# Kernel tuning notes

Measured on AMD Instinct MI355X. Metric: run time of the kernel, lower is better.

Reference implementation:

```python
import jax, jax.numpy as jnp
import numpy as np

STEP = 2
NEG = -1.0e10  # matches masked_fill_(-10000000000.0)


def leaky_relu(x):
    # nn.LeakyReLU(0.2)
    return jnp.where(x >= 0, x, 0.2 * x)


def setup_inputs() -> dict:
    key = jax.random.key(0)
    k1, k2, k3, k4 = jax.random.split(key, 4)
    B, E, N, H = 16, 1024, 1024, 128
    nodes_hidden = jax.random.normal(k1, (B, N, H), dtype=jnp.float32)
    # sparse-ish binary hyperedge incidence matrix (batch, edge_num, node_num)
    hn_adj = jax.random.bernoulli(k2, 0.1, (B, E, N)).astype(jnp.float32)
    # Linear(H+1, 1, bias=False) weights for q1 / q2, flattened to (H+1,)
    w1 = jax.random.normal(k3, (H + 1,), dtype=jnp.float32) / np.sqrt(H + 1).astype(np.float32)
    w2 = jax.random.normal(k4, (H + 1,), dtype=jnp.float32) / np.sqrt(H + 1).astype(np.float32)
    return {"nodes_hidden": nodes_hidden, "hn_adj": hn_adj, "w1": w1, "w2": w2}


def reference(nodes_hidden, hn_adj, w1, w2):
    # Dropout is inference-mode identity.
    H = nodes_hidden.shape[-1]
    # edge init: mean of incident node features
    deg = jnp.sum(hn_adj, axis=-1, keepdims=True)            # (B,E,1)
    deg = jnp.where(deg == 0.0, 1.0, deg)
    edge = jnp.matmul(hn_adj, nodes_hidden) / deg            # (B,E,H)
    nodes = nodes_hidden
    for _ in range(STEP):
        # q1(concat(edge*node, adj)) == (edge*node)@w1[:H] + adj*w1[H]
        # fused rank-1 score: never materialize (B,E,N,H)
        alpha = leaky_relu(
            jnp.einsum("bed,bnd,d->ben", edge, nodes, w1[:H]) + hn_adj * w1[H]
        )                                                     # (B,E,N)
        alpha = jnp.where(hn_adj == 0, NEG, alpha)
        alpha = jax.nn.softmax(alpha, axis=-1)
        edge = jnp.einsum("ben,bnd->bed", alpha, nodes)       # new edge hidden
        adj_t = jnp.swapaxes(hn_adj, 1, 2)                    # (B,N,E)
        beta = leaky_relu(
            jnp.einsum("bed,bnd,d->bne", edge, nodes, w2[:H]) + adj_t * w2[H]
        )                                                     # (B,N,E)
        beta = jnp.where(adj_t == 0, NEG, beta)
        beta = jax.nn.softmax(beta, axis=-1)
        nodes = jnp.einsum("bne,bed->bnd", beta, edge)        # new node hidden
    return (nodes, edge)
```

## Files before the change

kernel.cpp:

```cpp
#include <hip/hip_runtime.h>
#include <cstdint>
#include <cstddef>

#define B_ 16
#define E_ 1024
#define N_ 1024
#define H_ 128
#define CAP 192
#define NC 16
#define EC 64

typedef unsigned short u16;

#define UPK2(u, flo, fhi) \
    flo = __uint_as_float((u) << 16); fhi = __uint_as_float((u) & 0xffff0000u)

__device__ __forceinline__ u16 f2bf(float f) {
    unsigned u = __float_as_uint(f);
    return (u16)((u + 0x7fffu + ((u >> 16) & 1u)) >> 16);
}

__device__ __forceinline__ float wave_sum64(float v) {
    v += __shfl_xor(v, 32);
    v += __shfl_xor(v, 16);
    v += __shfl_xor(v, 8);
    v += __shfl_xor(v, 4);
    v += __shfl_xor(v, 2);
    v += __shfl_xor(v, 1);
    return v;
}

__global__ void build_rows(const float* __restrict__ adj,
                           u16* __restrict__ idx, int* __restrict__ cnt_out) {
    int be = blockIdx.x;
    const float* row = adj + (size_t)be * N_;
    __shared__ int wcnt[4];
    __shared__ int base;
    int tid = threadIdx.x, lane = tid & 63, wv = tid >> 6;
    if (tid == 0) base = 0;
    __syncthreads();
    for (int c0 = 0; c0 < N_; c0 += 256) {
        float v = row[c0 + tid];
        unsigned long long m = __ballot(v != 0.0f);
        if (lane == 0) wcnt[wv] = __popcll(m);
        __syncthreads();
        int pos = base;
        for (int w = 0; w < wv; ++w) pos += wcnt[w];
        pos += __popcll(m & ((1ull << lane) - 1ull));
        if (v != 0.0f && pos < CAP)
            idx[(size_t)be * CAP + pos] = (u16)(c0 + tid);
        __syncthreads();
        if (tid == 0) base += wcnt[0] + wcnt[1] + wcnt[2] + wcnt[3];
        __syncthreads();
    }
    if (tid == 0) cnt_out[be] = base < CAP ? base : CAP;
}

__global__ void col_count(const float* __restrict__ adj, int* __restrict__ cnt_chunk) {
    int blk = blockIdx.x;
    int ng = blk & 3;
    int c  = (blk >> 2) & (NC - 1);
    int b  = blk >> 6;
    int n = (ng << 8) + threadIdx.x;
    const float* base = adj + ((size_t)(b * E_ + c * EC)) * N_ + n;
    int cc = 0;
#pragma unroll 8
    for (int e = 0; e < EC; ++e)
        cc += (base[(size_t)e * N_] != 0.0f);
    cnt_chunk[(size_t)(b * NC + c) * N_ + n] = cc;
}

__global__ void col_prefix(const int* __restrict__ cnt_chunk,
                           int* __restrict__ off_chunk, int* __restrict__ cnt_out) {
    int idx = blockIdx.x * 256 + threadIdx.x;
    int b = idx >> 10, n = idx & 1023;
    int run = 0;
    for (int c = 0; c < NC; ++c) {
        size_t p = (size_t)(b * NC + c) * N_ + n;
        off_chunk[p] = run;
        run += cnt_chunk[p];
    }
    cnt_out[idx] = run < CAP ? run : CAP;
}

__global__ void col_place(const float* __restrict__ adj,
                          const int* __restrict__ off_chunk, u16* __restrict__ idx) {
    int blk = blockIdx.x;
    int ng = blk & 3;
    int c  = (blk >> 2) & (NC - 1);
    int b  = blk >> 6;
    int n = (ng << 8) + threadIdx.x;
    const float* base = adj + ((size_t)(b * E_ + c * EC)) * N_ + n;
    int pos = off_chunk[(size_t)(b * NC + c) * N_ + n];
    u16* lst = idx + ((size_t)b * N_ + n) * CAP;
    for (int e = 0; e < EC; ++e) {
        if (base[(size_t)e * N_] != 0.0f) {
            if (pos < CAP) lst[pos] = (u16)(c * EC + e);
            ++pos;
        }
    }
}

__global__ void to_bf16(const float* __restrict__ in, u16* __restrict__ out) {
    int i = blockIdx.x * 256 + threadIdx.x;
    float4 v = ((const float4*)in)[i];
    ushort4 r;
    r.x = f2bf(v.x); r.y = f2bf(v.y); r.z = f2bf(v.z); r.w = f2bf(v.w);
    ((ushort4*)out)[i] = r;
}

__global__ void edge_init(const u16* __restrict__ nodes_bf,
                          const u16* __restrict__ ridx, const int* __restrict__ rcnt,
                          float* __restrict__ edge) {
    int be = blockIdx.x;
    int b = be >> 10;
    int tid = threadIdx.x, d4 = tid & 31, h = tid >> 5;
    __shared__ u16 sidx[CAP];
    __shared__ float4 part4[256];
    int cnt = rcnt[be];
    for (int i = tid; i < cnt; i += 256) sidx[i] = ridx[(size_t)be * CAP + i];
    __syncthreads();
    const uint2* nb2 = (const uint2*)(nodes_bf + (size_t)b * N_ * H_);
    float4 acc = make_float4(0.f, 0.f, 0.f, 0.f);
    for (int i = h; i < cnt; i += 8) {
        uint2 u = nb2[(unsigned)sidx[i] * 32 + d4];
        float f0, f1, f2, f3;
        UPK2(u.x, f0, f1); UPK2(u.y, f2, f3);
        acc.x += f0; acc.y += f1; acc.z += f2; acc.w += f3;
    }
    part4[tid] = acc;
    __syncthreads();
    if (tid < 32) {
        float4 r = make_float4(0.f, 0.f, 0.f, 0.f);
#pragma unroll
        for (int k = 0; k < 8; ++k) {
            float4 p = part4[tid + (k << 5)];
            r.x += p.x; r.y += p.y; r.z += p.z; r.w += p.w;
        }
        float inv = 1.0f / (float)(cnt > 0 ? cnt : 1);
        r.x *= inv; r.y *= inv; r.z *= inv; r.w *= inv;
        ((float4*)edge)[(size_t)be * 32 + tid] = r;
    }
}

__global__ void __launch_bounds__(256, 4)
attn_gather(const float* __restrict__ qsrc,
            const u16* __restrict__ kv_bf,
            const float* __restrict__ w,
            const u16* __restrict__ lidx, const int* __restrict__ lcnt,
            float* __restrict__ out, u16* __restrict__ out_bf) {
    int x = blockIdx.x;
    int xcd = x & 7;
    int j = x >> 3;
    int b = xcd + ((j >> 8) << 3);
    int rg = (j & 255) << 2;
    int tid = threadIdx.x, lane = tid & 63, wv = tid >> 6;
    int br = (b << 10) + rg + wv;
    __shared__ u16 sidx[4][CAP];
    int cnt = lcnt[br];
    for (int i = lane; i < cnt; i += 64) sidx[wv][i] = lidx[(size_t)br * CAP + i];

    int esub = lane >> 3, dsub = lane & 7;
    const float4* qp = (const float4*)(qsrc + (size_t)br * H_);
    const float4* wp = (const float4*)w;
    float4 qr0, qr1, qr2, qr3;
    {
        float4 q0 = qp[(dsub << 2) + 0], w0 = wp[(dsub << 2) + 0];
        float4 q1 = qp[(dsub << 2) + 1], w1 = wp[(dsub << 2) + 1];
        float4 q2 = qp[(dsub << 2) + 2], w2 = wp[(dsub << 2) + 2];
        float4 q3 = qp[(dsub << 2) + 3], w3 = wp[(dsub << 2) + 3];
        const float L2E = 1.44269504f;
        qr0.x = q0.x * w0.x * L2E; qr0.y = q0.y * w0.y * L2E;
        qr0.z = q0.z * w0.z * L2E; qr0.w = q0.w * w0.w * L2E;
        qr1.x = q1.x * w1.x * L2E; qr1.y = q1.y * w1.y * L2E;
        qr1.z = q1.z * w1.z * L2E; qr1.w = q1.w * w1.w * L2E;
        qr2.x = q2.x * w2.x * L2E; qr2.y = q2.y * w2.y * L2E;
        qr2.z = q2.z * w2.z * L2E; qr2.w = q2.w * w2.w * L2E;
        qr3.x = q3.x * w3.x * L2E; qr3.y = q3.y * w3.y * L2E;
        qr3.z = q3.z * w3.z * L2E; qr3.w = q3.w * w3.w * L2E;
    }
    float wb = w[H_] * 1.44269504f;
    const uint4* kb4 = (const uint4*)(kv_bf + (size_t)b * 1024 * H_);

    float4 a0 = make_float4(0.f, 0.f, 0.f, 0.f);
    float4 a1 = a0, a2 = a0, a3 = a0;
    float dpart = 0.f;

    unsigned ro = (unsigned)((esub < cnt) ? sidx[wv][esub] : 0) * 16 + (dsub << 1);
    uint4 g0 = kb4[ro];
    uint4 g1 = kb4[ro + 1];

    for (int i0 = 0; i0 < cnt; i0 += 8) {
        int inx = i0 + 8 + esub;
        unsigned rn = (unsigned)((inx < cnt) ? sidx[wv][inx] : 0) * 16 + (dsub << 1);
        uint4 n0 = kb4[rn];
        uint4 n1 = kb4[rn + 1];
        int i = i0 + esub;
        float f0, f1, f2, f3, f4, f5, f6, f7;
        float f8, f9, f10, f11, f12, f13, f14, f15;
        UPK2(g0.x, f0, f1);   UPK2(g0.y, f2, f3);
        UPK2(g0.z, f4, f5);   UPK2(g0.w, f6, f7);
        UPK2(g1.x, f8, f9);   UPK2(g1.y, f10, f11);
        UPK2(g1.z, f12, f13); UPK2(g1.w, f14, f15);
        float dA = 0.f, dB = 0.f;
        dA = fmaf(f0, qr0.x, dA);  dB = fmaf(f1, qr0.y, dB);
        dA = fmaf(f2, qr0.z, dA);  dB = fmaf(f3, qr0.w, dB);
        dA = fmaf(f4, qr1.x, dA);  dB = fmaf(f5, qr1.y, dB);
        dA = fmaf(f6, qr1.z, dA);  dB = fmaf(f7, qr1.w, dB);
        dA = fmaf(f8, qr2.x, dA);  dB = fmaf(f9, qr2.y, dB);
        dA = fmaf(f10, qr2.z, dA); dB = fmaf(f11, qr2.w, dB);
        dA = fmaf(f12, qr3.x, dA); dB = fmaf(f13, qr3.y, dB);
        dA = fmaf(f14, qr3.z, dA); dB = fmaf(f15, qr3.w, dB);
        float d = dA + dB;
        d += __shfl_xor(d, 1);
        d += __shfl_xor(d, 2);
        d += __shfl_xor(d, 4);
        float p = d + wb;
        p = p >= 0.f ? p : 0.2f * p;
        float ww = (i < cnt) ? exp2f(p) : 0.f;
        dpart += ww;
        a0.x = fmaf(ww, f0, a0.x);  a0.y = fmaf(ww, f1, a0.y);
        a0.z = fmaf(ww, f2, a0.z);  a0.w = fmaf(ww, f3, a0.w);
        a1.x = fmaf(ww, f4, a1.x);  a1.y = fmaf(ww, f5, a1.y);
        a1.z = fmaf(ww, f6, a1.z);  a1.w = fmaf(ww, f7, a1.w);
        a2.x = fmaf(ww, f8, a2.x);  a2.y = fmaf(ww, f9, a2.y);
        a2.z = fmaf(ww, f10, a2.z); a2.w = fmaf(ww, f11, a2.w);
        a3.x = fmaf(ww, f12, a3.x); a3.y = fmaf(ww, f13, a3.y);
        a3.z = fmaf(ww, f14, a3.z); a3.w = fmaf(ww, f15, a3.w);
        g0 = n0; g1 = n1;
    }

#define RED3(f) f += __shfl_xor(f, 8); f += __shfl_xor(f, 16); f += __shfl_xor(f, 32)
    RED3(a0.x); RED3(a0.y); RED3(a0.z); RED3(a0.w);
    RED3(a1.x); RED3(a1.y); RED3(a1.z); RED3(a1.w);
    RED3(a2.x); RED3(a2.y); RED3(a2.z); RED3(a2.w);
    RED3(a3.x); RED3(a3.y); RED3(a3.z); RED3(a3.w);
#undef RED3
    float denom = wave_sum64(dpart) * 0.125f;
    float rden = denom > 0.f ? 1.0f / denom : 0.f;

    if (esub == 0) {
        a0.x *= rden; a0.y *= rden; a0.z *= rden; a0.w *= rden;
        a1.x *= rden; a1.y *= rden; a1.z *= rden; a1.w *= rden;
        a2.x *= rden; a2.y *= rden; a2.z *= rden; a2.w *= rden;
        a3.x *= rden; a3.y *= rden; a3.z *= rden; a3.w *= rden;
        float4* op = (float4*)out + (size_t)br * 32 + (dsub << 2);
        op[0] = a0; op[1] = a1; op[2] = a2; op[3] = a3;
        ushort4* hp = (ushort4*)out_bf + (size_t)br * 32 + (dsub << 2);
        ushort4 h0, h1, h2, h3;
        h0.x = f2bf(a0.x); h0.y = f2bf(a0.y); h0.z = f2bf(a0.z); h0.w = f2bf(a0.w);
        h1.x = f2bf(a1.x); h1.y = f2bf(a1.y); h1.z = f2bf(a1.z); h1.w = f2bf(a1.w);
        h2.x = f2bf(a2.x); h2.y = f2bf(a2.y); h2.z = f2bf(a2.z); h2.w = f2bf(a2.w);
        h3.x = f2bf(a3.x); h3.y = f2bf(a3.y); h3.z = f2bf(a3.z); h3.w = f2bf(a3.w);
        hp[0] = h0; hp[1] = h1; hp[2] = h2; hp[3] = h3;
    }
}

extern "C" void kernel_launch(void* const* d_in, const int* in_sizes, int n_in,
                              void* d_out, int out_size, void* d_ws, size_t ws_size,
                              hipStream_t stream) {
    const float* nodes_in = (const float*)d_in[0];
    const float* adj      = (const float*)d_in[1];
    const float* w1       = (const float*)d_in[2];
    const float* w2       = (const float*)d_in[3];

    char* ws = (char*)d_ws;
    size_t off = 0;
    u16* row_idx = (u16*)(ws + off); off += (size_t)B_ * E_ * CAP * sizeof(u16);
    u16* col_idx = (u16*)(ws + off); off += (size_t)B_ * N_ * CAP * sizeof(u16);
    int* row_cnt = (int*)(ws + off); off += (size_t)B_ * E_ * sizeof(int);
    int* col_cnt = (int*)(ws + off); off += (size_t)B_ * N_ * sizeof(int);
    int* cnt_chunk = (int*)(ws + off); off += (size_t)B_ * NC * N_ * sizeof(int);
    int* off_chunk = (int*)(ws + off); off += (size_t)B_ * NC * N_ * sizeof(int);
    u16* nodes_bf = (u16*)(ws + off); off += (size_t)B_ * N_ * H_ * sizeof(u16);
    u16* edge_bf  = (u16*)(ws + off); off += (size_t)B_ * E_ * H_ * sizeof(u16);

    float* out_nodes = (float*)d_out;
    float* out_edge  = out_nodes + (size_t)B_ * N_ * H_;

    build_rows<<<dim3(B_ * E_), dim3(256), 0, stream>>>(adj, row_idx, row_cnt);
    col_count <<<dim3(B_ * NC * 4), dim3(256), 0, stream>>>(adj, cnt_chunk);
    col_prefix<<<dim3(B_ * N_ / 256), dim3(256), 0, stream>>>(cnt_chunk, off_chunk, col_cnt);
    col_place <<<dim3(B_ * NC * 4), dim3(256), 0, stream>>>(adj, off_chunk, col_idx);
    to_bf16   <<<dim3(B_ * N_ * H_ / 1024), dim3(256), 0, stream>>>(nodes_in, nodes_bf);
    edge_init <<<dim3(B_ * E_), dim3(256), 0, stream>>>(nodes_bf, row_idx, row_cnt, out_edge);

    const float* ncur = nodes_in;
    for (int s = 0; s < 2; ++s) {
        attn_gather<<<dim3(B_ * E_ / 4), dim3(256), 0, stream>>>(
            out_edge, nodes_bf, w1, row_idx, row_cnt, out_edge, edge_bf);
        attn_gather<<<dim3(B_ * N_ / 4), dim3(256), 0, stream>>>(
            ncur, edge_bf, w2, col_idx, col_cnt, out_nodes, nodes_bf);
        ncur = out_nodes;
    }
}
```

Before: 267.6 us.

## Rework edge_init as wave-per-row gather, finer column chunks, skip final bf16 write

```diff
diff --git a/kernel.cpp b/kernel.cpp
--- a/kernel.cpp
+++ b/kernel.cpp
@@ -7,8 +7,8 @@
 #define N_ 1024
 #define H_ 128
 #define CAP 192
-#define NC 16
-#define EC 64
+#define NC 32
+#define EC 32
 
 typedef unsigned short u16;
 
@@ -60,7 +60,7 @@
     int blk = blockIdx.x;
     int ng = blk & 3;
     int c  = (blk >> 2) & (NC - 1);
-    int b  = blk >> 6;
+    int b  = blk >> 7;
     int n = (ng << 8) + threadIdx.x;
     const float* base = adj + ((size_t)(b * E_ + c * EC)) * N_ + n;
     int cc = 0;
@@ -88,7 +88,7 @@
     int blk = blockIdx.x;
     int ng = blk & 3;
     int c  = (blk >> 2) & (NC - 1);
-    int b  = blk >> 6;
+    int b  = blk >> 7;
     int n = (ng << 8) + threadIdx.x;
     const float* base = adj + ((size_t)(b * E_ + c * EC)) * N_ + n;
     int pos = off_chunk[(size_t)(b * NC + c) * N_ + n];
@@ -109,37 +109,68 @@
     ((ushort4*)out)[i] = r;
 }
 
-__global__ void edge_init(const u16* __restrict__ nodes_bf,
-                          const u16* __restrict__ ridx, const int* __restrict__ rcnt,
-                          float* __restrict__ edge) {
-    int be = blockIdx.x;
-    int b = be >> 10;
-    int tid = threadIdx.x, d4 = tid & 31, h = tid >> 5;
-    __shared__ u16 sidx[CAP];
-    __shared__ float4 part4[256];
+__global__ void __launch_bounds__(256, 4)
+edge_init(const u16* __restrict__ nodes_bf,
+          const u16* __restrict__ ridx, const int* __restrict__ rcnt,
+          float* __restrict__ edge) {
+    int x = blockIdx.x;
+    int xcd = x & 7;
+    int j = x >> 3;
+    int b = xcd + ((j >> 8) << 3);
+    int rg = (j & 255) << 2;
+    int tid = threadIdx.x, lane = tid & 63, wv = tid >> 6;
+    int be = (b << 10) + rg + wv;
+    __shared__ u16 sidx[4][CAP];
     int cnt = rcnt[be];
-    for (int i = tid; i < cnt; i += 256) sidx[i] = ridx[(size_t)be * CAP + i];
-    __syncthreads();
-    const uint2* nb2 = (const uint2*)(nodes_bf + (size_t)b * N_ * H_);
-    float4 acc = make_float4(0.f, 0.f, 0.f, 0.f);
-    for (int i = h; i < cnt; i += 8) {
-        uint2 u = nb2[(unsigned)sidx[i] * 32 + d4];
-        float f0, f1, f2, f3;
-        UPK2(u.x, f0, f1); UPK2(u.y, f2, f3);
-        acc.x += f0; acc.y += f1; acc.z += f2; acc.w += f3;
-    }
-    part4[tid] = acc;
-    __syncthreads();
-    if (tid < 32) {
-        float4 r = make_float4(0.f, 0.f, 0.f, 0.f);
-#pragma unroll
-        for (int k = 0; k < 8; ++k) {
-            float4 p = part4[tid + (k << 5)];
-            r.x += p.x; r.y += p.y; r.z += p.z; r.w += p.w;
-        }
+    for (int i = lane; i < cnt; i += 64) sidx[wv][i] = ridx[(size_t)be * CAP + i];
+
+    int esub = lane >> 3, dsub = lane & 7;
+    const uint4* kb4 = (const uint4*)(nodes_bf + (size_t)b * N_ * H_);
+    float4 a0 = make_float4(0.f, 0.f, 0.f, 0.f);
+    float4 a1 = a0, a2 = a0, a3 = a0;
+
+    unsigned ro = (unsigned)((esub < cnt) ? sidx[wv][esub] : 0) * 16 + (dsub << 1);
+    uint4 g0 = kb4[ro];
+    uint4 g1 = kb4[ro + 1];
+
+    for (int i0 = 0; i0 < cnt; i0 += 8) {
+        int inx = i0 + 8 + esub;
+        unsigned rn = (unsigned)((inx < cnt) ? sidx[wv][inx] : 0) * 16 + (dsub << 1);
+        uint4 n0 = kb4[rn];
+        uint4 n1 = kb4[rn + 1];
+        int i = i0 + esub;
+        float f0, f1, f2, f3, f4, f5, f6, f7;
+        float f8, f9, f10, f11, f12, f13, f14, f15;
+        UPK2(g0.x, f0, f1);   UPK2(g0.y, f2, f3);
+        UPK2(g0.z, f4, f5);   UPK2(g0.w, f6, f7);
+        UPK2(g1.x, f8, f9);   UPK2(g1.y, f10, f11);
+        UPK2(g1.z, f12, f13); UPK2(g1.w, f14, f15);
+        float ww = (i < cnt) ? 1.0f : 0.f;
+        a0.x = fmaf(ww, f0, a0.x);  a0.y = fmaf(ww, f1, a0.y);
+        a0.z = fmaf(ww, f2, a0.z);  a0.w = fmaf(ww, f3, a0.w);
+        a1.x = fmaf(ww, f4, a1.x);  a1.y = fmaf(ww, f5, a1.y);
+        a1.z = fmaf(ww, f6, a1.z);  a1.w = fmaf(ww, f7, a1.w);
+        a2.x = fmaf(ww, f8, a2.x);  a2.y = fmaf(ww, f9, a2.y);
+        a2.z = fmaf(ww, f10, a2.z); a2.w = fmaf(ww, f11, a2.w);
+        a3.x = fmaf(ww, f12, a3.x); a3.y = fmaf(ww, f13, a3.y);
+        a3.z = fmaf(ww, f14, a3.z); a3.w = fmaf(ww, f15, a3.w);
+        g0 = n0; g1 = n1;
+    }
+
+#define RED3(f) f += __shfl_xor(f, 8); f += __shfl_xor(f, 16); f += __shfl_xor(f, 32)
+    RED3(a0.x); RED3(a0.y); RED3(a0.z); RED3(a0.w);
+    RED3(a1.x); RED3(a1.y); RED3(a1.z); RED3(a1.w);
+    RED3(a2.x); RED3(a2.y); RED3(a2.z); RED3(a2.w);
+    RED3(a3.x); RED3(a3.y); RED3(a3.z); RED3(a3.w);
+#undef RED3
+    if (esub == 0) {
         float inv = 1.0f / (float)(cnt > 0 ? cnt : 1);
-        r.x *= inv; r.y *= inv; r.z *= inv; r.w *= inv;
-        ((float4*)edge)[(size_t)be * 32 + tid] = r;
+        a0.x *= inv; a0.y *= inv; a0.z *= inv; a0.w *= inv;
+        a1.x *= inv; a1.y *= inv; a1.z *= inv; a1.w *= inv;
+        a2.x *= inv; a2.y *= inv; a2.z *= inv; a2.w *= inv;
+        a3.x *= inv; a3.y *= inv; a3.z *= inv; a3.w *= inv;
+        float4* op = (float4*)edge + (size_t)be * 32 + (dsub << 2);
+        op[0] = a0; op[1] = a1; op[2] = a2; op[3] = a3;
     }
 }
 
@@ -148,7 +179,7 @@
             const u16* __restrict__ kv_bf,
             const float* __restrict__ w,
             const u16* __restrict__ lidx, const int* __restrict__ lcnt,
-            float* __restrict__ out, u16* __restrict__ out_bf) {
+            float* __restrict__ out, u16* __restrict__ out_bf, int wbf) {
     int x = blockIdx.x;
     int xcd = x & 7;
     int j = x >> 3;
@@ -246,13 +277,15 @@
         a3.x *= rden; a3.y *= rden; a3.z *= rden; a3.w *= rden;
         float4* op = (float4*)out + (size_t)br * 32 + (dsub << 2);
         op[0] = a0; op[1] = a1; op[2] = a2; op[3] = a3;
-        ushort4* hp = (ushort4*)out_bf + (size_t)br * 32 + (dsub << 2);
-        ushort4 h0, h1, h2, h3;
-        h0.x = f2bf(a0.x); h0.y = f2bf(a0.y); h0.z = f2bf(a0.z); h0.w = f2bf(a0.w);
-        h1.x = f2bf(a1.x); h1.y = f2bf(a1.y); h1.z = f2bf(a1.z); h1.w = f2bf(a1.w);
-        h2.x = f2bf(a2.x); h2.y = f2bf(a2.y); h2.z = f2bf(a2.z); h2.w = f2bf(a2.w);
-        h3.x = f2bf(a3.x); h3.y = f2bf(a3.y); h3.z = f2bf(a3.z); h3.w = f2bf(a3.w);
-        hp[0] = h0; hp[1] = h1; hp[2] = h2; hp[3] = h3;
+        if (wbf) {
+            ushort4* hp = (ushort4*)out_bf + (size_t)br * 32 + (dsub << 2);
+            ushort4 h0, h1, h2, h3;
+            h0.x = f2bf(a0.x); h0.y = f2bf(a0.y); h0.z = f2bf(a0.z); h0.w = f2bf(a0.w);
+            h1.x = f2bf(a1.x); h1.y = f2bf(a1.y); h1.z = f2bf(a1.z); h1.w = f2bf(a1.w);
+            h2.x = f2bf(a2.x); h2.y = f2bf(a2.y); h2.z = f2bf(a2.z); h2.w = f2bf(a2.w);
+            h3.x = f2bf(a3.x); h3.y = f2bf(a3.y); h3.z = f2bf(a3.z); h3.w = f2bf(a3.w);
+            hp[0] = h0; hp[1] = h1; hp[2] = h2; hp[3] = h3;
+        }
     }
 }
 
@@ -283,14 +316,14 @@
     col_prefix<<<dim3(B_ * N_ / 256), dim3(256), 0, stream>>>(cnt_chunk, off_chunk, col_cnt);
     col_place <<<dim3(B_ * NC * 4), dim3(256), 0, stream>>>(adj, off_chunk, col_idx);
     to_bf16   <<<dim3(B_ * N_ * H_ / 1024), dim3(256), 0, stream>>>(nodes_in, nodes_bf);
-    edge_init <<<dim3(B_ * E_), dim3(256), 0, stream>>>(nodes_bf, row_idx, row_cnt, out_edge);
+    edge_init <<<dim3(B_ * E_ / 4), dim3(256), 0, stream>>>(nodes_bf, row_idx, row_cnt, out_edge);
 
     const float* ncur = nodes_in;
     for (int s = 0; s < 2; ++s) {
         attn_gather<<<dim3(B_ * E_ / 4), dim3(256), 0, stream>>>(
-            out_edge, nodes_bf, w1, row_idx, row_cnt, out_edge, edge_bf);
+            out_edge, nodes_bf, w1, row_idx, row_cnt, out_edge, edge_bf, 1);
         attn_gather<<<dim3(B_ * N_ / 4), dim3(256), 0, stream>>>(
-            ncur, edge_bf, w2, col_idx, col_cnt, out_nodes, nodes_bf);
+            ncur, edge_bf, w2, col_idx, col_cnt, out_nodes, nodes_bf, s == 0 ? 1 : 0);
         ncur = out_nodes;
     }
 }
```

Result: faster. 232.8 us (-13.0%).
